# Kernel optimization log

Measured on AMD Instinct MI355X. Metric: run time of the kernel, lower is better.

The kernel has to match this reference:

```python
import jax, jax.numpy as jnp
import numpy as np

IN_FEATURES = 512
DIM_EXPLOSION = 20
OUT_FEATURES = IN_FEATURES * DIM_EXPLOSION  # 10240
NB_PROJ_ENTRIES = 6
HASH_LENGTH = 32
BATCH = 4096


def _make_sparse_proj(key):
    """Sparse binary random projection: each of the OUT_FEATURES rows has
    NB_PROJ_ENTRIES entries set to 1 (as in OlfactoryModel.create_rand_proj_matrix)."""
    idx = jax.random.randint(key, (OUT_FEATURES, NB_PROJ_ENTRIES), 0, IN_FEATURES)
    rows = jnp.arange(OUT_FEATURES)[:, None]
    W = jnp.zeros((OUT_FEATURES, IN_FEATURES), dtype=jnp.float32)
    return W.at[rows, idx].set(1.0)


def setup_inputs() -> dict:
    key = jax.random.key(0)
    k1, k2 = jax.random.split(key)
    inp = jax.random.uniform(k1, (BATCH, IN_FEATURES), dtype=jnp.float32)
    W = _make_sparse_proj(k2)
    return {"input": inp, "weight": W, "hash_length": HASH_LENGTH}


def reference(input, weight, hash_length):
    # F.linear: [B, in] @ [out, in]^T -> [B, out]
    x = jnp.einsum('bi,oi->bo', input, weight)
    # MB_sparsify: winner-take-all, keep top `hash_length` activations per row, zero the rest
    topv = jax.lax.top_k(x, hash_length)[0]          # [B, k]
    thresh = topv[:, -1:]                            # k-th largest per row
    return jnp.where(x >= thresh, x, jnp.zeros_like(x))
```

## Files before the change

kernel.cpp:

```cpp
#include <hip/hip_runtime.h>


typedef float f4 __attribute__((ext_vector_type(4)));

constexpr int IN_F   = 512;
constexpr int OUT_F  = 10240;
constexpr int TPB    = 1024;
constexpr int ROWS   = 4;
constexpr int FPT    = OUT_F / TPB;
constexpr int NBINS  = 1024;
constexpr int NWAVES = TPB / 64;
constexpr int CAP    = 64;

static_assert(NBINS == 64 * 16, "wave scan assumes 16 bins per lane");

__global__ __launch_bounds__(256) void extract_idx(const float* __restrict__ W,
                                                   uint4* __restrict__ packed,
                                                   int out_f) {
  int row  = blockIdx.x * 4 + (threadIdx.x >> 6);
  int lane = threadIdx.x & 63;
  if (row >= out_f) return;

  const float* wr = W + (size_t)row * IN_F;
  unsigned long long masks[8];
#pragma unroll
  for (int c = 0; c < 8; ++c) {
    float v = wr[c * 64 + lane];
    masks[c] = __ballot(v != 0.0f);
  }
  if (lane == 0) {
    unsigned idx[6] = {IN_F, IN_F, IN_F, IN_F, IN_F, IN_F};
    int n = 0;
#pragma unroll
    for (int c = 0; c < 8; ++c) {
      unsigned long long m = masks[c];
      while (m && n < 6) {
        int b = __builtin_ctzll(m);
        idx[n++] = (unsigned)(c * 64 + b);
        m &= m - 1;
      }
    }
    uint4 r;
    r.x = idx[0] | (idx[1] << 16);
    r.y = idx[2] | (idx[3] << 16);
    r.z = idx[4] | (idx[5] << 16);
    r.w = (unsigned)n;
    packed[row] = r;
  }
}

__device__ __forceinline__ float row_val(const f4* in4, uint4 p, int r) {
  const float* b = (const float*)in4;
  float s = b[(p.x & 0xFFFFu) * 4 + r];
  s += b[(p.x >> 16) * 4 + r];
  s += b[(p.y & 0xFFFFu) * 4 + r];
  s += b[(p.y >> 16) * 4 + r];
  s += b[(p.z & 0xFFFFu) * 4 + r];
  s += b[(p.z >> 16) * 4 + r];
  return s;
}

__global__ __launch_bounds__(TPB, 4) void fly_hash(const float* __restrict__ inp,
                                                   const uint4* __restrict__ packed,
                                                   const int* __restrict__ kptr,
                                                   float* __restrict__ out) {
  __shared__ f4    in4[IN_F + 1];
  __shared__ int   hist[ROWS * NBINS];
  __shared__ int   wsum[NWAVES];
  __shared__ int   sh_bstar[ROWS], sh_above[ROWS], sh_n[ROWS], sh_cnt[ROWS];
  __shared__ float sh_list[ROWS][CAP];
  __shared__ float sh_thr[ROWS];
  __shared__ int   sh_need[ROWS];

  const int tid  = threadIdx.x;
  const int lane = tid & 63;
  const int wid  = tid >> 6;
  const int row0 = blockIdx.x * ROWS;
  const int k    = *kptr;

  if (tid < IN_F) {
    const float* p = inp + (size_t)row0 * IN_F + tid;
    f4 v;
    v.x = p[0];
    v.y = p[IN_F];
    v.z = p[2 * IN_F];
    v.w = p[3 * IN_F];
    in4[tid] = v;
  } else if (tid == IN_F) {
    f4 z = {0.0f, 0.0f, 0.0f, 0.0f};
    in4[IN_F] = z;
  }
  if (tid < ROWS) { sh_bstar[tid] = -1; sh_cnt[tid] = 0; }
  for (int i = tid; i < ROWS * NBINS; i += TPB) hist[i] = 0;
  __syncthreads();

  f4 x4[FPT];
#pragma unroll
  for (int i = 0; i < FPT; ++i) {
    uint4 r = packed[tid + i * TPB];
    f4 s = in4[r.x & 0xFFFFu];
    s += in4[r.x >> 16];
    s += in4[r.y & 0xFFFFu];
    s += in4[r.y >> 16];
    s += in4[r.z & 0xFFFFu];
    s += in4[r.z >> 16];
    x4[i] = s;
#pragma unroll
    for (int rr = 0; rr < ROWS; ++rr) {
      float v = s[rr];
      if (v >= 4.0f) {
        int b = (int)((v - 4.0f) * 512.0f);
        b = b > NBINS - 1 ? NBINS - 1 : b;
        atomicAdd(&hist[rr * NBINS + b], 1);
      }
    }
  }
  __syncthreads();

  if (wid < ROWS) {
    const int r = wid;
    const int base = r * NBINS + lane * 16;
    int csum = 0;
#pragma unroll
    for (int j = 0; j < 16; ++j) csum += hist[base + j];
    int s = csum;
#pragma unroll
    for (int off = 1; off < 64; off <<= 1) {
      int t = __shfl_down(s, off);
      if (lane + off < 64) s += t;
    }
    int s_next = __shfl_down(s, 1);
    if (lane == 63) s_next = 0;
    if (s >= k && s_next < k) {
      int acc = s_next;
      int bsel = lane * 16, abv = s_next;
      for (int b = lane * 16 + 15; b >= lane * 16; --b) {
        int h = hist[r * NBINS + b];
        if (acc + h >= k) { bsel = b; abv = acc; break; }
        acc += h;
      }
      sh_bstar[r] = bsel;
      sh_above[r] = abv;
      sh_n[r]     = hist[r * NBINS + bsel];
    }
  }
  __syncthreads();

  {
    const int b0 = sh_bstar[0], b1 = sh_bstar[1];
    const int b2 = sh_bstar[2], b3 = sh_bstar[3];
#pragma unroll
    for (int i = 0; i < FPT; ++i) {
      f4 s = x4[i];
#pragma unroll
      for (int rr = 0; rr < ROWS; ++rr) {
        float v = s[rr];
        int bb = (rr == 0) ? b0 : (rr == 1) ? b1 : (rr == 2) ? b2 : b3;
        if (v >= 4.0f) {
          int b = (int)((v - 4.0f) * 512.0f);
          b = b > NBINS - 1 ? NBINS - 1 : b;
          if (b == bb) {
            int p = atomicAdd(&sh_cnt[rr], 1);
            if (p < CAP) sh_list[rr][p] = v;
          }
        }
      }
    }
  }
  __syncthreads();

  if (wid < ROWS) {
    const int r   = wid;
    const int bst = sh_bstar[r];
    const int n   = (bst >= 0) ? sh_n[r] : CAP + 1;
    if (bst >= 0 && n <= CAP && sh_cnt[r] <= CAP) {
      const int j = k - sh_above[r];
      float vl = (lane < n) ? sh_list[r][lane] : -1.0f;
      int cgt = 0, cge = 0;
      for (int m = 0; m < n; ++m) {
        float u = sh_list[r][m];
        cgt += (u > vl);
        cge += (u >= vl);
      }
      if (lane < n && cgt < j && cge >= j) sh_thr[r] = vl;
      if (lane == 0) sh_need[r] = 0;
    } else {
      if (lane == 0) sh_need[r] = 1;
    }
  }
  __syncthreads();

#pragma unroll 1
  for (int r = 0; r < ROWS; ++r) {
    if (!sh_need[r]) continue;
    unsigned lo = 0u, hi = __float_as_uint(8.0f);
    while (lo < hi) {
      unsigned mid = lo + ((hi - lo + 1u) >> 1);
      float fm = __uint_as_float(mid);
      int c = 0;
      for (int i = 0; i < FPT; ++i) {
        uint4 p = packed[tid + i * TPB];
        c += (int)__popcll(__ballot(row_val(in4, p, r) >= fm));
      }
      if (lane == 0) wsum[wid] = c;
      __syncthreads();
      int tot = 0;
#pragma unroll
      for (int w = 0; w < NWAVES; ++w) tot += wsum[w];
      if (tot >= k) lo = mid; else hi = mid - 1u;
      __syncthreads();
    }
    if (tid == 0) sh_thr[r] = __uint_as_float(lo);
    __syncthreads();
  }
  const float t0 = sh_thr[0];
  const float t1 = sh_thr[1];
  const float t2 = sh_thr[2];
  const float t3 = sh_thr[3];

  float* o0 = out + (size_t)(row0 + 0) * OUT_F;
  float* o1 = out + (size_t)(row0 + 1) * OUT_F;
  float* o2 = out + (size_t)(row0 + 2) * OUT_F;
  float* o3 = out + (size_t)(row0 + 3) * OUT_F;
#pragma unroll
  for (int i = 0; i < FPT; ++i) {
    int f = tid + i * TPB;
    f4 v = x4[i];
    __builtin_nontemporal_store((v.x >= t0) ? v.x : 0.0f, &o0[f]);
    __builtin_nontemporal_store((v.y >= t1) ? v.y : 0.0f, &o1[f]);
    __builtin_nontemporal_store((v.z >= t2) ? v.z : 0.0f, &o2[f]);
    __builtin_nontemporal_store((v.w >= t3) ? v.w : 0.0f, &o3[f]);
  }
}

extern "C" void kernel_launch(void* const* d_in, const int* in_sizes, int n_in,
                              void* d_out, int out_size, void* d_ws, size_t ws_size,
                              hipStream_t stream) {
  const float* inp = (const float*)d_in[0];
  const float* W   = (const float*)d_in[1];
  const int* kptr  = (const int*)d_in[2];
  float* out       = (float*)d_out;

  const int batch = in_sizes[0] / IN_F;
  const int out_f = in_sizes[1] / IN_F;

  uint4* packed = (uint4*)d_ws;

  hipLaunchKernelGGL(extract_idx, dim3((out_f + 3) / 4), dim3(256), 0, stream,
                     W, packed, out_f);
  hipLaunchKernelGGL(fly_hash, dim3(batch / ROWS), dim3(TPB), 0, stream,
                     inp, packed, kptr, out);
}
```

Before: 238.6 us.

## Replace shared histogram top-k selection with fixed-cut candidate list and wave-local refinement

Drops the 4096-bin shared histogram, the second pass over the activations and the extra block barriers. Values at or above a fixed cutoff of 4.5 now go straight into a per-row candidate list of up to 256 entries. One wave per row then bins that list into 64 buckets, prefix-scans to find the threshold bucket and ranks the values in that bucket with shuffles. If fewer than k values pass the cut, or the list overflows, the row falls back to the existing bitwise binary search, which is expensive. The fixed cutoff is tuned to the value distribution of the test inputs.

```diff
diff --git a/kernel.cpp b/kernel.cpp
--- a/kernel.cpp
+++ b/kernel.cpp
@@ -8,11 +8,9 @@
 constexpr int TPB    = 1024;
 constexpr int ROWS   = 4;
 constexpr int FPT    = OUT_F / TPB;
-constexpr int NBINS  = 1024;
 constexpr int NWAVES = TPB / 64;
-constexpr int CAP    = 64;
-
-static_assert(NBINS == 64 * 16, "wave scan assumes 16 bins per lane");
+constexpr int CAP    = 256;
+constexpr float CUT  = 4.5f;
 
 __global__ __launch_bounds__(256) void extract_idx(const float* __restrict__ W,
                                                    uint4* __restrict__ packed,
@@ -65,9 +63,8 @@
                                                    const int* __restrict__ kptr,
                                                    float* __restrict__ out) {
   __shared__ f4    in4[IN_F + 1];
-  __shared__ int   hist[ROWS * NBINS];
   __shared__ int   wsum[NWAVES];
-  __shared__ int   sh_bstar[ROWS], sh_above[ROWS], sh_n[ROWS], sh_cnt[ROWS];
+  __shared__ int   sh_cnt[ROWS];
   __shared__ float sh_list[ROWS][CAP];
   __shared__ float sh_thr[ROWS];
   __shared__ int   sh_need[ROWS];
@@ -90,8 +87,7 @@
     f4 z = {0.0f, 0.0f, 0.0f, 0.0f};
     in4[IN_F] = z;
   }
-  if (tid < ROWS) { sh_bstar[tid] = -1; sh_cnt[tid] = 0; }
-  for (int i = tid; i < ROWS * NBINS; i += TPB) hist[i] = 0;
+  if (tid < ROWS) sh_cnt[tid] = 0;
   __syncthreads();
 
   f4 x4[FPT];
@@ -108,10 +104,9 @@
 #pragma unroll
     for (int rr = 0; rr < ROWS; ++rr) {
       float v = s[rr];
-      if (v >= 4.0f) {
-        int b = (int)((v - 4.0f) * 512.0f);
-        b = b > NBINS - 1 ? NBINS - 1 : b;
-        atomicAdd(&hist[rr * NBINS + b], 1);
+      if (v >= CUT) {
+        int p = atomicAdd(&sh_cnt[rr], 1);
+        if (p < CAP) sh_list[rr][p] = v;
       }
     }
   }
@@ -119,74 +114,53 @@
 
   if (wid < ROWS) {
     const int r = wid;
-    const int base = r * NBINS + lane * 16;
-    int csum = 0;
-#pragma unroll
-    for (int j = 0; j < 16; ++j) csum += hist[base + j];
-    int s = csum;
-#pragma unroll
-    for (int off = 1; off < 64; off <<= 1) {
-      int t = __shfl_down(s, off);
-      if (lane + off < 64) s += t;
-    }
-    int s_next = __shfl_down(s, 1);
-    if (lane == 63) s_next = 0;
-    if (s >= k && s_next < k) {
-      int acc = s_next;
-      int bsel = lane * 16, abv = s_next;
-      for (int b = lane * 16 + 15; b >= lane * 16; --b) {
-        int h = hist[r * NBINS + b];
-        if (acc + h >= k) { bsel = b; abv = acc; break; }
-        acc += h;
-      }
-      sh_bstar[r] = bsel;
-      sh_above[r] = abv;
-      sh_n[r]     = hist[r * NBINS + bsel];
-    }
-  }
-  __syncthreads();
-
-  {
-    const int b0 = sh_bstar[0], b1 = sh_bstar[1];
-    const int b2 = sh_bstar[2], b3 = sh_bstar[3];
-#pragma unroll
-    for (int i = 0; i < FPT; ++i) {
-      f4 s = x4[i];
-#pragma unroll
-      for (int rr = 0; rr < ROWS; ++rr) {
-        float v = s[rr];
-        int bb = (rr == 0) ? b0 : (rr == 1) ? b1 : (rr == 2) ? b2 : b3;
-        if (v >= 4.0f) {
-          int b = (int)((v - 4.0f) * 512.0f);
-          b = b > NBINS - 1 ? NBINS - 1 : b;
-          if (b == bb) {
-            int p = atomicAdd(&sh_cnt[rr], 1);
-            if (p < CAP) sh_list[rr][p] = v;
-          }
-        }
-      }
-    }
-  }
-  __syncthreads();
-
-  if (wid < ROWS) {
-    const int r   = wid;
-    const int bst = sh_bstar[r];
-    const int n   = (bst >= 0) ? sh_n[r] : CAP + 1;
-    if (bst >= 0 && n <= CAP && sh_cnt[r] <= CAP) {
-      const int j = k - sh_above[r];
-      float vl = (lane < n) ? sh_list[r][lane] : -1.0f;
-      int cgt = 0, cge = 0;
+    const int n = sh_cnt[r];
+    int need = 1;
+    if (n >= k && n <= CAP) {
+      int cnt = 0;
       for (int m = 0; m < n; ++m) {
         float u = sh_list[r][m];
-        cgt += (u > vl);
-        cge += (u >= vl);
-      }
-      if (lane < n && cgt < j && cge >= j) sh_thr[r] = vl;
-      if (lane == 0) sh_need[r] = 0;
-    } else {
-      if (lane == 0) sh_need[r] = 1;
-    }
+        int b = (int)((u - CUT) * 32.0f);
+        b = b > 63 ? 63 : b;
+        cnt += (b == lane);
+      }
+      int s = cnt;
+#pragma unroll
+      for (int off = 1; off < 64; off <<= 1) {
+        int t = __shfl_down(s, off);
+        if (lane + off < 64) s += t;
+      }
+      int s_next = __shfl_down(s, 1);
+      if (lane == 63) s_next = 0;
+      bool cross = (s >= k) && (s_next < k);
+      unsigned long long cm = __ballot(cross);
+      int cl = (int)__builtin_ctzll(cm);
+      int bsel  = cl;
+      int above = __shfl(s_next, cl);
+      float vl = -1.0f;
+      int m2 = 0;
+      for (int m = 0; m < n; ++m) {
+        float u = sh_list[r][m];
+        int b = (int)((u - CUT) * 32.0f);
+        b = b > 63 ? 63 : b;
+        if (b == bsel) {
+          if (lane == m2) vl = u;
+          ++m2;
+        }
+      }
+      if (m2 <= 64) {
+        const int j = k - above;
+        int cgt = 0, cge = 0;
+        for (int i = 0; i < m2; ++i) {
+          float u = __shfl(vl, i);
+          cgt += (u > vl);
+          cge += (u >= vl);
+        }
+        if (lane < m2 && cgt < j && cge >= j) sh_thr[r] = vl;
+        need = 0;
+      }
+    }
+    if (lane == 0) sh_need[r] = need;
   }
   __syncthreads();
 
```

Result: slower. 638.3 us (+167.5%).
